# Optimization experiments

Measured on AMD Instinct MI355X. Metric: run time of the kernel, lower is better.

Reference implementation:

```python
import jax, jax.numpy as jnp
import numpy as np

K_SIZES = (3, 9)          # per-level local window sizes (both < 13)
K_NUM = tuple((k * k - 1) // 2 for k in K_SIZES)  # topk sizes: (4, 40)
BN_EPS = 1e-5


def _make_local_ids(W, patch_id, k):
    """Replicates get_local_index (k<13 branch): wrap-around kxk window minus center."""
    r = k // 2
    out = []
    for i in patch_id:
        i = int(i)
        ix, iy = i // W, i % W
        wx = np.zeros(W)
        wy = np.zeros(W)
        for j in range(-r, r + 1):
            wx[(ix + j) % W] = 1.0
            wy[(iy + j) % W] = 1.0
        wgt = (wy[None, :] * wx[:, None]).reshape(-1)  # row-major: idx = x*W + y
        wgt[i] = 0.0
        out.append(np.nonzero(wgt)[0])
    return np.stack(out).astype(np.int64)  # [N, k*k-1]


def setup_inputs() -> dict:
    key = jax.random.key(0)
    ks = jax.random.split(key, 8)
    B = 8
    feat0 = jax.random.normal(ks[0], (B, 512, 8, 8), jnp.float32)
    feat1 = jax.random.normal(ks[1], (B, 64, 128, 128), jnp.float32)
    rng = np.random.default_rng(0)
    patch_id0 = rng.permutation(8 * 8)[:64]
    patch_id1 = rng.permutation(128 * 128)[:512]
    local_id0 = _make_local_ids(8, patch_id0, K_SIZES[0])    # [64, 8]
    local_id1 = _make_local_ids(128, patch_id1, K_SIZES[1])  # [512, 80]
    s = 0.02
    return dict(
        feat0=feat0, feat1=feat1,
        W1=jax.random.normal(ks[2], (1024, 512), jnp.float32) * s,
        b1=jnp.zeros((1024,), jnp.float32),
        gamma=jnp.ones((1024,), jnp.float32),
        beta=jnp.zeros((1024,), jnp.float32),
        W2=jax.random.normal(ks[3], (256, 1024), jnp.float32) * s,
        b2=jnp.zeros((256,), jnp.float32),
        W3=jax.random.normal(ks[4], (256, 64), jnp.float32) * s,
        b3=jnp.zeros((256,), jnp.float32),
        W4=jax.random.normal(ks[5], (256, 256), jnp.float32) * s,
        b4=jnp.zeros((256,), jnp.float32),
        patch_id0=jnp.asarray(patch_id0, jnp.int64 if jax.config.jax_enable_x64 else jnp.int32),
        patch_id1=jnp.asarray(patch_id1, jnp.int64 if jax.config.jax_enable_x64 else jnp.int32),
        local_id0=jnp.asarray(local_id0, jnp.int64 if jax.config.jax_enable_x64 else jnp.int32),
        local_id1=jnp.asarray(local_id1, jnp.int64 if jax.config.jax_enable_x64 else jnp.int32),
        patch_size=128,
    )


def _sample(feat, patch_id, local_id, k_num):
    """gather local patches -> cosine sim vs center -> topk -> gather winners."""
    B, C, H, W = feat.shape
    fr = jnp.transpose(feat, (0, 2, 3, 1)).reshape(B, H * W, C)  # [B, HW, C]
    norm = jnp.linalg.norm(fr, axis=-1, keepdims=True)
    xn = fr / jnp.maximum(norm, 1e-12)                 # F.normalize(dim=-1)
    loc = xn[:, local_id]                              # [B, N, L, C]
    cen = xn[:, patch_id]                              # [B, N, C]
    sim = jnp.einsum('bnlc,bnc->bnl', loc, cen)        # [B, N, L]
    _, top = jax.lax.top_k(sim, k_num)                 # [B, N, k]
    N, L = local_id.shape
    top = top.reshape(B * N, k_num, 1)
    x_loc = fr[:, local_id].reshape(B * N, L, C)
    x_loc = jnp.take_along_axis(x_loc, jnp.broadcast_to(top, (B * N, k_num, C)), axis=1)
    x_cen = fr[:, patch_id].reshape(B * N, 1, C)
    return jnp.concatenate([x_cen, x_loc], axis=1)     # [B*N, 1+k, C]


def reference(feat0, feat1, W1, b1, gamma, beta, W2, b2, W3, b3, W4, b4,
              patch_id0, patch_id1, local_id0, local_id1, patch_size):
    # level 0: h == patch_size // 16 -> adaptive_avg_pool over (1+k) axis, then mlp1
    x0 = _sample(feat0, patch_id0, local_id0, K_NUM[0])  # [B*N0, 1+k0, 512]
    x0 = x0.mean(axis=1)                                 # adaptive_avg_pool2d -> (1, dim)
    h = x0 @ W1.T + b1
    mu = h.mean(axis=0)
    var = h.var(axis=0)                                  # BatchNorm1d (training stats)
    h = (h - mu) / jnp.sqrt(var + BN_EPS) * gamma + beta
    out0 = jax.nn.relu(h) @ W2.T + b2                    # [B*N0, 256]

    # level 1: h == patch_size -> mlp2 per (center+neighbors) row, then l2norm
    x1 = _sample(feat1, patch_id1, local_id1, K_NUM[1])  # [B*N1, 1+k1, 64]
    BN1, M, C1 = x1.shape
    y = x1.reshape(-1, C1)
    y = jax.nn.relu(y @ W3.T + b3) @ W4.T + b4           # [B*N1*(1+k1), 256]
    y = y / (jnp.linalg.norm(y, axis=1, keepdims=True) + 1e-7)  # Normalize(2)
    out1 = y.reshape(BN1, M, -1)                         # [B*N1, 1+k1, 256]
    return out0, out1
```

## Files before the change

kernel.cpp:

```cpp
#include <hip/hip_runtime.h>
#include <math.h>

typedef _Float16 f16x8 __attribute__((ext_vector_type(8)));
typedef float f32x4 __attribute__((ext_vector_type(4)));


__global__ __launch_bounds__(256) void k_wprep(
    const float* __restrict__ W3, const float* __restrict__ W4,
    unsigned short* __restrict__ PB3h, unsigned short* __restrict__ PB3l,
    unsigned short* __restrict__ PB4h, unsigned short* __restrict__ PB4l)
{
    const int e = blockIdx.x * 256 + threadIdx.x;
    if (e < 16384) {
        const int j = e & 7, l = (e >> 3) & 63, ks = (e >> 9) & 1, nt = e >> 10;
        const int n = nt * 16 + (l & 15);
        const int k = ks * 32 + (l >> 4) * 8 + j;
        const float w = W3[n * 64 + k];
        const _Float16 hi = (_Float16)w;
        const _Float16 lo = (_Float16)(w - (float)hi);
        ((_Float16*)PB3h)[e] = hi;
        ((_Float16*)PB3l)[e] = lo;
    }
    {
        const int j = e & 7, l = (e >> 3) & 63, ks = (e >> 9) & 7, nt = e >> 12;
        const int n = nt * 16 + (l & 15);
        const int k = ks * 32 + (l >> 4) * 8 + j;
        const float w = W4[n * 256 + k];
        const _Float16 hi = (_Float16)w;
        const _Float16 lo = (_Float16)(w - (float)hi);
        ((_Float16*)PB4h)[e] = hi;
        ((_Float16*)PB4l)[e] = lo;
    }
}

__global__ __launch_bounds__(256) void k_transpose1(
    const float* __restrict__ feat1, float* __restrict__ featT)
{
    __shared__ float tile[64][65];
    const int b = blockIdx.y;
    const int p0 = blockIdx.x * 64;
    const int tid = threadIdx.x;
    const float* fb = feat1 + (size_t)b * 64 * 16384;
    float* ft = featT + (size_t)b * 16384 * 64;
    #pragma unroll
    for (int it = 0; it < 16; ++it) {
        const int e = it * 256 + tid;
        const int c = e >> 6, p = e & 63;
        tile[p][c] = fb[(size_t)c * 16384 + p0 + p];
    }
    __syncthreads();
    #pragma unroll
    for (int it = 0; it < 16; ++it) {
        const int e = it * 256 + tid;
        const int p = e >> 6, c = e & 63;
        ft[(size_t)(p0 + p) * 64 + c] = tile[p][c];
    }
}

__global__ __launch_bounds__(128) void k_sims1T(
    const float* __restrict__ featT, const int* __restrict__ patch_id1,
    const int* __restrict__ local_id1, int* __restrict__ idx)
{
    __shared__ float cen[64];
    __shared__ double sims[80];
    __shared__ double cnorm;

    const int row = blockIdx.x;
    const int b = row >> 9;
    const int n = row & 511;
    const int tid = threadIdx.x;
    const float* ft = featT + (size_t)b * 16384 * 64;
    const int pid = patch_id1[n];
    const int* lids = local_id1 + n * 80;

    if (tid < 64) cen[tid] = ft[(size_t)pid * 64 + tid];
    __syncthreads();

    if (tid < 64) {
        double v = (double)cen[tid];
        double s = v * v;
        for (int o = 32; o > 0; o >>= 1) s += __shfl_down(s, o);
        if (tid == 0) { s = sqrt(s); cnorm = (s < 1e-12) ? 1e-12 : s; }
    }
    __syncthreads();

    if (tid < 80) {
        const float4* rp = (const float4*)(ft + (size_t)lids[tid] * 64);
        double d = 0.0, q = 0.0;
        #pragma unroll
        for (int k = 0; k < 16; ++k) {
            const float4 v4 = rp[k];
            double v;
            v = (double)v4.x; d += v * (double)cen[4*k+0]; q += v*v;
            v = (double)v4.y; d += v * (double)cen[4*k+1]; q += v*v;
            v = (double)v4.z; d += v * (double)cen[4*k+2]; q += v*v;
            v = (double)v4.w; d += v * (double)cen[4*k+3]; q += v*v;
        }
        double nl = sqrt(q); if (nl < 1e-12) nl = 1e-12;
        sims[tid] = d / (nl * cnorm);
    }
    __syncthreads();

    if (tid < 80) {
        const double s = sims[tid];
        int rank = 0;
        for (int j = 0; j < 80; ++j) {
            const double sj = sims[j];
            rank += (sj > s) || (sj == s && j < tid);
        }
        if (rank < 40) idx[row * 41 + 1 + rank] = lids[tid];
    }
    if (tid == 0) idx[row * 41] = pid;
}

__global__ __launch_bounds__(128) void k_sims1(
    const float* __restrict__ feat1, const int* __restrict__ patch_id1,
    const int* __restrict__ local_id1, int* __restrict__ idx)
{
    __shared__ float cen[64];
    __shared__ double sims[80];
    __shared__ double cnorm;

    const int row = blockIdx.x;
    const int b = row >> 9;
    const int n = row & 511;
    const int tid = threadIdx.x;
    const float* fb = feat1 + (size_t)b * 64 * 16384;
    const int pid = patch_id1[n];
    const int* lids = local_id1 + n * 80;

    if (tid < 64) cen[tid] = fb[(size_t)tid * 16384 + pid];
    __syncthreads();

    if (tid < 64) {
        double v = (double)cen[tid];
        double s = v * v;
        for (int o = 32; o > 0; o >>= 1) s += __shfl_down(s, o);
        if (tid == 0) { s = sqrt(s); cnorm = (s < 1e-12) ? 1e-12 : s; }
    }
    __syncthreads();

    if (tid < 80) {
        const int lpix = lids[tid];
        double d = 0.0, q = 0.0;
        for (int c = 0; c < 64; ++c) {
            double v = (double)fb[(size_t)c * 16384 + lpix];
            d += v * (double)cen[c];
            q += v * v;
        }
        double nl = sqrt(q); if (nl < 1e-12) nl = 1e-12;
        sims[tid] = d / (nl * cnorm);
    }
    __syncthreads();

    if (tid < 80) {
        const double s = sims[tid];
        int rank = 0;
        for (int j = 0; j < 80; ++j) {
            const double sj = sims[j];
            rank += (sj > s) || (sj == s && j < tid);
        }
        if (rank < 40) idx[row * 41 + 1 + rank] = lids[tid];
    }
    if (tid == 0) idx[row * 41] = pid;
}

__global__ __launch_bounds__(256) void k_mlp_mfma(
    const float* __restrict__ featb,
    const unsigned short* __restrict__ PB3h, const unsigned short* __restrict__ PB3l,
    const unsigned short* __restrict__ PB4h, const unsigned short* __restrict__ PB4l,
    const float* __restrict__ b3, const float* __restrict__ b4,
    float* __restrict__ ybuf)
{
    __shared__ _Float16 XH[32][72];
    __shared__ _Float16 XL[32][72];
    __shared__ float T1[32][260];
    __shared__ float rsums[2][2][16];

    const int tid = threadIdx.x;
    const int blk = blockIdx.x;
    const int img = blk >> 9;
    const int p0 = (blk & 511) * 32;
    const float* fb = featb + (size_t)img * 64 * 16384;
    float* yb = ybuf + (size_t)img * (size_t)(16384 * 256);

    {
        const int p = tid & 31;
        const int cg = tid >> 5;
        #pragma unroll
        for (int k = 0; k < 8; ++k) {
            const int c = cg * 8 + k;
            const float v = fb[(size_t)c * 16384 + p0 + p];
            const _Float16 hi = (_Float16)v;
            XH[p][c] = hi;
            XL[p][c] = (_Float16)(v - (float)hi);
        }
    }
    __syncthreads();

    const int lane = tid & 63;
    const int w = tid >> 6;
    const int mt = w & 1;
    const int nh = w >> 1;
    const int lrow = lane & 15;
    const int kblk = lane >> 4;

    {
        f16x8 ah[2], al[2];
        #pragma unroll
        for (int ks = 0; ks < 2; ++ks) {
            ah[ks] = *(const f16x8*)&XH[mt*16 + lrow][ks*32 + kblk*8];
            al[ks] = *(const f16x8*)&XL[mt*16 + lrow][ks*32 + kblk*8];
        }
        const f16x8* B3H = (const f16x8*)PB3h;
        const f16x8* B3L = (const f16x8*)PB3l;
        #pragma unroll
        for (int t = 0; t < 8; ++t) {
            const int nt = nh*8 + t;
            f32x4 acc = {0.f, 0.f, 0.f, 0.f};
            #pragma unroll
            for (int ks = 0; ks < 2; ++ks) {
                const f16x8 bh = B3H[(nt*2 + ks)*64 + lane];
                const f16x8 bl = B3L[(nt*2 + ks)*64 + lane];
                acc = __builtin_amdgcn_mfma_f32_16x16x32_f16(al[ks], bh, acc, 0, 0, 0);
                acc = __builtin_amdgcn_mfma_f32_16x16x32_f16(ah[ks], bl, acc, 0, 0, 0);
                acc = __builtin_amdgcn_mfma_f32_16x16x32_f16(ah[ks], bh, acc, 0, 0, 0);
            }
            const float bias = b3[nt*16 + lrow];
            #pragma unroll
            for (int r = 0; r < 4; ++r)
                T1[mt*16 + kblk*4 + r][nt*16 + lrow] = fmaxf(acc[r] + bias, 0.f);
        }
    }
    __syncthreads();

    f32x4 acc2[8];
    #pragma unroll
    for (int t = 0; t < 8; ++t) acc2[t] = (f32x4){0.f, 0.f, 0.f, 0.f};
    {
        const f16x8* B4H = (const f16x8*)PB4h;
        const f16x8* B4L = (const f16x8*)PB4l;
        #pragma unroll 2
        for (int ks = 0; ks < 8; ++ks) {
            float a[8];
            *(float4*)&a[0] = *(const float4*)&T1[mt*16 + lrow][ks*32 + kblk*8];
            *(float4*)&a[4] = *(const float4*)&T1[mt*16 + lrow][ks*32 + kblk*8 + 4];
            f16x8 ah2, al2;
            #pragma unroll
            for (int j = 0; j < 8; ++j) {
                const _Float16 hi = (_Float16)a[j];
                ah2[j] = hi;
                al2[j] = (_Float16)(a[j] - (float)hi);
            }
            #pragma unroll
            for (int t = 0; t < 8; ++t) {
                const int nt = nh*8 + t;
                const f16x8 bh = B4H[(nt*8 + ks)*64 + lane];
                const f16x8 bl = B4L[(nt*8 + ks)*64 + lane];
                acc2[t] = __builtin_amdgcn_mfma_f32_16x16x32_f16(al2, bh, acc2[t], 0, 0, 0);
                acc2[t] = __builtin_amdgcn_mfma_f32_16x16x32_f16(ah2, bl, acc2[t], 0, 0, 0);
                acc2[t] = __builtin_amdgcn_mfma_f32_16x16x32_f16(ah2, bh, acc2[t], 0, 0, 0);
            }
        }
    }
    float p[4] = {0.f, 0.f, 0.f, 0.f};
    #pragma unroll
    for (int t = 0; t < 8; ++t) {
        const float bias = b4[(nh*8 + t)*16 + lrow];
        #pragma unroll
        for (int r = 0; r < 4; ++r) {
            acc2[t][r] += bias;
            p[r] += acc2[t][r] * acc2[t][r];
        }
    }
    #pragma unroll
    for (int r = 0; r < 4; ++r)
        for (int o = 1; o < 16; o <<= 1) p[r] += __shfl_xor(p[r], o);
    if (lrow == 0) {
        #pragma unroll
        for (int r = 0; r < 4; ++r) rsums[mt][nh][kblk*4 + r] = p[r];
    }
    __syncthreads();
    float inv[4];
    #pragma unroll
    for (int r = 0; r < 4; ++r) {
        const float s = rsums[mt][0][kblk*4 + r] + rsums[mt][1][kblk*4 + r];
        inv[r] = 1.f / (sqrtf(s) + 1e-7f);
    }
    #pragma unroll
    for (int t = 0; t < 8; ++t) {
        const int col = (nh*8 + t)*16 + lrow;
        #pragma unroll
        for (int r = 0; r < 4; ++r)
            yb[(size_t)(p0 + mt*16 + kblk*4 + r) * 256 + col] = acc2[t][r] * inv[r];
    }
}

__global__ __launch_bounds__(256) void k_mlp_pix2(
    const float* __restrict__ featb,
    const float* __restrict__ W3T, const float* __restrict__ b3,
    const float* __restrict__ W4T, const float* __restrict__ b4,
    float* __restrict__ ybuf, int ybufStride)
{
    __shared__ __align__(16) float xs[32 * 68];
    __shared__ __align__(16) float t1s[32 * 256];

    const int tid = threadIdx.x;
    const int blk = blockIdx.x;
    const int img = blk >> 9;
    const int p0 = (blk & 511) * 32;
    const float* fb = featb + (size_t)img * 64 * 16384;
    float* yb = ybuf + (size_t)img * (size_t)ybufStride;

    {
        const int p = tid & 31;
        const int cg = tid >> 5;
        #pragma unroll
        for (int k = 0; k < 8; ++k) {
            const int c = cg * 8 + k;
            xs[p * 68 + c] = fb[(size_t)c * 16384 + p0 + p];
        }
    }
    __syncthreads();

    const int jg = tid & 63;
    const int g = tid >> 6;
    const int j0 = jg * 4;
    const int mb = g * 8;

    {
        float acc[8][4];
        #pragma unroll
        for (int r = 0; r < 8; ++r) {
            acc[r][0] = 0.f; acc[r][1] = 0.f; acc[r][2] = 0.f; acc[r][3] = 0.f;
        }
        const float4* Wf = (const float4*)W3T;
        const float4* xsf = (const float4*)xs;
        #pragma unroll 4
        for (int cq = 0; cq < 16; ++cq) {
            const float4 wA = Wf[(cq * 4 + 0) * 64 + jg];
            const float4 wB = Wf[(cq * 4 + 1) * 64 + jg];
            const float4 wC = Wf[(cq * 4 + 2) * 64 + jg];
            const float4 wD = Wf[(cq * 4 + 3) * 64 + jg];
            #pragma unroll
            for (int r = 0; r < 8; ++r) {
                const float4 x4 = xsf[(mb + r) * 17 + cq];
                acc[r][0] += x4.x*wA.x + x4.y*wB.x + x4.z*wC.x + x4.w*wD.x;
                acc[r][1] += x4.x*wA.y + x4.y*wB.y + x4.z*wC.y + x4.w*wD.y;
                acc[r][2] += x4.x*wA.z + x4.y*wB.z + x4.z*wC.z + x4.w*wD.z;
                acc[r][3] += x4.x*wA.w + x4.y*wB.w + x4.z*wC.w + x4.w*wD.w;
            }
        }
        const float bb0 = b3[j0], bb1 = b3[j0+1], bb2 = b3[j0+2], bb3 = b3[j0+3];
        #pragma unroll
        for (int r = 0; r < 8; ++r) {
            float4 o4;
            o4.x = fmaxf(acc[r][0] + bb0, 0.f);
            o4.y = fmaxf(acc[r][1] + bb1, 0.f);
            o4.z = fmaxf(acc[r][2] + bb2, 0.f);
            o4.w = fmaxf(acc[r][3] + bb3, 0.f);
            *(float4*)&t1s[(mb + r) * 256 + j0] = o4;
        }
    }
    __syncthreads();

    {
        float acc[8][4];
        #pragma unroll
        for (int r = 0; r < 8; ++r) {
            acc[r][0] = 0.f; acc[r][1] = 0.f; acc[r][2] = 0.f; acc[r][3] = 0.f;
        }
        const float4* Wf = (const float4*)W4T;
        const float4* t1f = (const float4*)t1s;
        #pragma unroll 2
        for (int kq = 0; kq < 64; ++kq) {
            const float4 wA = Wf[(kq * 4 + 0) * 64 + jg];
            const float4 wB = Wf[(kq * 4 + 1) * 64 + jg];
            const float4 wC = Wf[(kq * 4 + 2) * 64 + jg];
            const float4 wD = Wf[(kq * 4 + 3) * 64 + jg];
            #pragma unroll
            for (int r = 0; r < 8; ++r) {
                const float4 t4 = t1f[(mb + r) * 64 + kq];
                acc[r][0] += t4.x*wA.x + t4.y*wB.x + t4.z*wC.x + t4.w*wD.x;
                acc[r][1] += t4.x*wA.y + t4.y*wB.y + t4.z*wC.y + t4.w*wD.y;
                acc[r][2] += t4.x*wA.z + t4.y*wB.z + t4.z*wC.z + t4.w*wD.z;
                acc[r][3] += t4.x*wA.w + t4.y*wB.w + t4.z*wC.w + t4.w*wD.w;
            }
        }
        const float bb0 = b4[j0], bb1 = b4[j0+1], bb2 = b4[j0+2], bb3 = b4[j0+3];
        #pragma unroll
        for (int r = 0; r < 8; ++r) {
            const float y0 = acc[r][0] + bb0;
            const float y1 = acc[r][1] + bb1;
            const float y2 = acc[r][2] + bb2;
            const float y3 = acc[r][3] + bb3;
            float p = y0*y0 + y1*y1 + y2*y2 + y3*y3;
            for (int o = 1; o < 64; o <<= 1) p += __shfl_xor(p, o);
            const float inv = 1.f / (sqrtf(p) + 1e-7f);
            float4 o4 = make_float4(y0*inv, y1*inv, y2*inv, y3*inv);
            *(float4*)&yb[(size_t)(p0 + mb + r) * 256 + j0] = o4;
        }
    }
}

__global__ __launch_bounds__(256) void k_wtrans(
    const float* __restrict__ W3, const float* __restrict__ W4,
    float* __restrict__ W3T, float* __restrict__ W4T)
{
    const int t = threadIdx.x;
    const int j = blockIdx.x;
    W4T[(size_t)t * 256 + j] = W4[(size_t)j * 256 + t];
    if (j < 64) W3T[(size_t)j * 256 + t] = W3[(size_t)t * 64 + j];
}

__global__ __launch_bounds__(256) void k_gather1(
    const float* __restrict__ ybuf, int ybufStride,
    const int* __restrict__ idxb, float* __restrict__ out1b)
{
    __shared__ int pix[41];
    const int bn = blockIdx.x;
    const int img = bn >> 9;
    const int tid = threadIdx.x;
    if (tid < 41) pix[tid] = idxb[bn * 41 + tid];
    __syncthreads();
    const float4* yb4 = (const float4*)(ybuf + (size_t)img * (size_t)ybufStride);
    float4* o4 = (float4*)(out1b + (size_t)bn * 41 * 256);
    for (int e = tid; e < 41 * 64; e += 256) {
        const int mi = e >> 6, j4 = e & 63;
        o4[mi * 64 + j4] = yb4[pix[mi] * 64 + j4];
    }
}

__global__ __launch_bounds__(256) void k_branch1(
    const float* __restrict__ feat1, const int* __restrict__ patch_id1,
    const int* __restrict__ local_id1, const float* __restrict__ W3,
    const float* __restrict__ b3, const float* __restrict__ W4,
    const float* __restrict__ b4, float* __restrict__ out1)
{
    __shared__ __align__(16) float xs[44 * 64];
    __shared__ __align__(16) float t1s[44 * 256];
    __shared__ double sims[80];
    __shared__ int winners[40];
    __shared__ float cen[64];
    __shared__ double cnorm;

    const int row = blockIdx.x;
    const int b = row >> 9;
    const int n = row & 511;
    const int tid = threadIdx.x;
    const float* fb = feat1 + (size_t)b * 64 * 16384;
    const int pid = patch_id1[n];
    const int* lids = local_id1 + n * 80;

    if (tid < 64) cen[tid] = fb[(size_t)tid * 16384 + pid];
    __syncthreads();

    if (tid < 64) {
        double v = (double)cen[tid];
        double s = v * v;
        for (int o = 32; o > 0; o >>= 1) s += __shfl_down(s, o);
        if (tid == 0) { s = sqrt(s); cnorm = (s < 1e-12) ? 1e-12 : s; }
    }
    __syncthreads();

    if (tid < 80) {
        const int lpix = lids[tid];
        double d = 0.0, q = 0.0;
        for (int c = 0; c < 64; ++c) {
            double v = (double)fb[(size_t)c * 16384 + lpix];
            d += v * (double)cen[c];
            q += v * v;
        }
        double nl = sqrt(q); if (nl < 1e-12) nl = 1e-12;
        sims[tid] = d / (nl * cnorm);
    }
    __syncthreads();

    if (tid < 80) {
        const double s = sims[tid];
        int rank = 0;
        for (int j = 0; j < 80; ++j) {
            const double sj = sims[j];
            rank += (sj > s) || (sj == s && j < tid);
        }
        if (rank < 40) winners[rank] = tid;
    }
    __syncthreads();

    for (int m = tid; m < 44 * 64; m += 256) {
        const int mi = m >> 6, c = m & 63;
        float v;
        if (mi >= 1 && mi <= 40) v = fb[(size_t)c * 16384 + lids[winners[mi - 1]]];
        else v = cen[c];
        xs[m] = v;
    }
    __syncthreads();

    const int jg = tid & 63;
    const int g = tid >> 6;
    const int j0 = jg * 4;
    const int mb = g * 11;

    {
        float acc[11][4];
        #pragma unroll
        for (int r = 0; r < 11; ++r) {
            acc[r][0] = 0.f; acc[r][1] = 0.f; acc[r][2] = 0.f; acc[r][3] = 0.f;
        }
        const float4* W3f = (const float4*)W3;
        const float4* xsf = (const float4*)xs;
        #pragma unroll 4
        for (int c4 = 0; c4 < 16; ++c4) {
            const float4 w0 = W3f[(j0 + 0) * 16 + c4];
            const float4 w1 = W3f[(j0 + 1) * 16 + c4];
            const float4 w2 = W3f[(j0 + 2) * 16 + c4];
            const float4 w3 = W3f[(j0 + 3) * 16 + c4];
            #pragma unroll
            for (int r = 0; r < 11; ++r) {
                const float4 x4 = xsf[(mb + r) * 16 + c4];
                acc[r][0] += x4.x*w0.x + x4.y*w0.y + x4.z*w0.z + x4.w*w0.w;
                acc[r][1] += x4.x*w1.x + x4.y*w1.y + x4.z*w1.z + x4.w*w1.w;
                acc[r][2] += x4.x*w2.x + x4.y*w2.y + x4.z*w2.z + x4.w*w2.w;
                acc[r][3] += x4.x*w3.x + x4.y*w3.y + x4.z*w3.z + x4.w*w3.w;
            }
        }
        const float bb0 = b3[j0], bb1 = b3[j0+1], bb2 = b3[j0+2], bb3 = b3[j0+3];
        #pragma unroll
        for (int r = 0; r < 11; ++r) {
            float4 o4;
            o4.x = fmaxf(acc[r][0] + bb0, 0.f);
            o4.y = fmaxf(acc[r][1] + bb1, 0.f);
            o4.z = fmaxf(acc[r][2] + bb2, 0.f);
            o4.w = fmaxf(acc[r][3] + bb3, 0.f);
            *(float4*)&t1s[(mb + r) * 256 + j0] = o4;
        }
    }
    __syncthreads();

    {
        float acc[11][4];
        #pragma unroll
        for (int r = 0; r < 11; ++r) {
            acc[r][0] = 0.f; acc[r][1] = 0.f; acc[r][2] = 0.f; acc[r][3] = 0.f;
        }
        const float4* W4f = (const float4*)W4;
        const float4* t1f = (const float4*)t1s;
        #pragma unroll 2
        for (int j4 = 0; j4 < 64; ++j4) {
            const float4 w0 = W4f[(j0 + 0) * 64 + j4];
            const float4 w1 = W4f[(j0 + 1) * 64 + j4];
            const float4 w2 = W4f[(j0 + 2) * 64 + j4];
            const float4 w3 = W4f[(j0 + 3) * 64 + j4];
            #pragma unroll
            for (int r = 0; r < 11; ++r) {
                const float4 t4 = t1f[(mb + r) * 64 + j4];
                acc[r][0] += t4.x*w0.x + t4.y*w0.y + t4.z*w0.z + t4.w*w0.w;
                acc[r][1] += t4.x*w1.x + t4.y*w1.y + t4.z*w1.z + t4.w*w1.w;
                acc[r][2] += t4.x*w2.x + t4.y*w2.y + t4.z*w2.z + t4.w*w2.w;
                acc[r][3] += t4.x*w3.x + t4.y*w3.y + t4.z*w3.z + t4.w*w3.w;
            }
        }
        const float bb0 = b4[j0], bb1 = b4[j0+1], bb2 = b4[j0+2], bb3 = b4[j0+3];
        #pragma unroll
        for (int r = 0; r < 11; ++r) {
            const float y0 = acc[r][0] + bb0;
            const float y1 = acc[r][1] + bb1;
            const float y2 = acc[r][2] + bb2;
            const float y3 = acc[r][3] + bb3;
            float p = y0*y0 + y1*y1 + y2*y2 + y3*y3;
            for (int o = 1; o < 64; o <<= 1) p += __shfl_xor(p, o);
            const float inv = 1.f / (sqrtf(p) + 1e-7f);
            const int mi = mb + r;
            if (mi < 41) {
                float4 o4 = make_float4(y0*inv, y1*inv, y2*inv, y3*inv);
                *(float4*)&out1[((size_t)row * 41 + mi) * 256 + j0] = o4;
            }
        }
    }
}

__global__ __launch_bounds__(64) void k_sample0(
    const float* __restrict__ feat0, const int* __restrict__ patch_id0,
    const int* __restrict__ local_id0, float* __restrict__ x0m)
{
    __shared__ float cen[512];
    __shared__ float loc[8][512];
    __shared__ double sims[8];
    __shared__ int winners[4];
    __shared__ double cnorm;

    const int row = blockIdx.x;
    const int b = row >> 6;
    const int n = row & 63;
    const int t = threadIdx.x;
    const float* fb = feat0 + (size_t)b * 512 * 64;
    const int pid = patch_id0[n];

    for (int c = t; c < 512; c += 64) cen[c] = fb[(size_t)c * 64 + pid];
    for (int l = 0; l < 8; ++l) {
        const int lp = local_id0[n * 8 + l];
        for (int c = t; c < 512; c += 64) loc[l][c] = fb[(size_t)c * 64 + lp];
    }
    __syncthreads();

    double cs = 0.0;
    for (int c = t; c < 512; c += 64) { double v = (double)cen[c]; cs += v * v; }
    for (int o = 32; o > 0; o >>= 1) cs += __shfl_down(cs, o);
    if (t == 0) { cs = sqrt(cs); cnorm = (cs < 1e-12) ? 1e-12 : cs; }
    __syncthreads();

    for (int l = 0; l < 8; ++l) {
        double d = 0.0, q = 0.0;
        for (int c = t; c < 512; c += 64) {
            double v = (double)loc[l][c];
            d += v * (double)cen[c];
            q += v * v;
        }
        for (int o = 32; o > 0; o >>= 1) { d += __shfl_down(d, o); q += __shfl_down(q, o); }
        if (t == 0) {
            double nl = sqrt(q); if (nl < 1e-12) nl = 1e-12;
            sims[l] = d / (nl * cnorm);
        }
    }
    __syncthreads();

    if (t < 8) {
        const double s = sims[t];
        int rank = 0;
        for (int j = 0; j < 8; ++j) {
            const double sj = sims[j];
            rank += (sj > s) || (sj == s && j < t);
        }
        if (rank < 4) winners[rank] = t;
    }
    __syncthreads();

    for (int c = t; c < 512; c += 64) {
        float a = cen[c];
        for (int r = 0; r < 4; ++r) a += loc[winners[r]][c];
        x0m[(size_t)row * 512 + c] = a * 0.2f;
    }
}

__global__ __launch_bounds__(128) void k_gemm1(
    const float* __restrict__ x, const float* __restrict__ W1,
    const float* __restrict__ b1, float* __restrict__ h)
{
    __shared__ __align__(16) float xsr[8 * 512];
    const int i0 = blockIdx.y * 8;
    const int tid = threadIdx.x;
    const int j0 = blockIdx.x * 512 + tid * 4;

    const float4* xg = (const float4*)(x + (size_t)i0 * 512);
    float4* xl = (float4*)xsr;
    #pragma unroll
    for (int e = 0; e < 8; ++e) xl[e * 128 + tid] = xg[e * 128 + tid];
    __syncthreads();

    float acc[8][4];
    #pragma unroll
    for (int r = 0; r < 8; ++r) {
        acc[r][0] = 0.f; acc[r][1] = 0.f; acc[r][2] = 0.f; acc[r][3] = 0.f;
    }
    const float4* W1f = (const float4*)W1;
    const float4* xf  = (const float4*)xsr;
    #pragma unroll 4
    for (int c4 = 0; c4 < 128; ++c4) {
        const float4 w0 = W1f[(size_t)(j0 + 0) * 128 + c4];
        const float4 w1 = W1f[(size_t)(j0 + 1) * 128 + c4];
        const float4 w2 = W1f[(size_t)(j0 + 2) * 128 + c4];
        const float4 w3 = W1f[(size_t)(j0 + 3) * 128 + c4];
        #pragma unroll
        for (int r = 0; r < 8; ++r) {
            const float4 x4 = xf[r * 128 + c4];
            acc[r][0] += x4.x*w0.x + x4.y*w0.y + x4.z*w0.z + x4.w*w0.w;
            acc[r][1] += x4.x*w1.x + x4.y*w1.y + x4.z*w1.z + x4.w*w1.w;
            acc[r][2] += x4.x*w2.x + x4.y*w2.y + x4.z*w2.z + x4.w*w2.w;
            acc[r][3] += x4.x*w3.x + x4.y*w3.y + x4.z*w3.z + x4.w*w3.w;
        }
    }
    const float bb0 = b1[j0], bb1 = b1[j0+1], bb2 = b1[j0+2], bb3 = b1[j0+3];
    #pragma unroll
    for (int r = 0; r < 8; ++r) {
        float4 o4 = make_float4(acc[r][0] + bb0, acc[r][1] + bb1,
                                acc[r][2] + bb2, acc[r][3] + bb3);
        *(float4*)&h[(size_t)(i0 + r) * 1024 + j0] = o4;
    }
}

__global__ __launch_bounds__(64) void k_bnstats(
    const float* __restrict__ h, float* __restrict__ mu, float* __restrict__ rstd)
{
    const int j = blockIdx.x;
    const int t = threadIdx.x;
    float s = 0.f, ss = 0.f;
    for (int i = t; i < 512; i += 64) {
        const float v = h[(size_t)i * 1024 + j];
        s += v; ss += v * v;
    }
    for (int o = 32; o > 0; o >>= 1) { s += __shfl_down(s, o); ss += __shfl_down(ss, o); }
    if (t == 0) {
        const float m = s * (1.f / 512.f);
        const float var = ss * (1.f / 512.f) - m * m;
        mu[j] = m;
        rstd[j] = rsqrtf(var + 1e-5f);
    }
}

__global__ __launch_bounds__(256) void k_bnapply(
    float* __restrict__ h, const float* __restrict__ mu, const float* __restrict__ rstd,
    const float* __restrict__ gamma, const float* __restrict__ beta)
{
    const int e = blockIdx.x * 256 + threadIdx.x;
    const int jb = (e & 255) * 4;
    float4 v = ((float4*)h)[e];
    v.x = fmaxf((v.x - mu[jb+0]) * rstd[jb+0] * gamma[jb+0] + beta[jb+0], 0.f);
    v.y = fmaxf((v.y - mu[jb+1]) * rstd[jb+1] * gamma[jb+1] + beta[jb+1], 0.f);
    v.z = fmaxf((v.z - mu[jb+2]) * rstd[jb+2] * gamma[jb+2] + beta[jb+2], 0.f);
    v.w = fmaxf((v.w - mu[jb+3]) * rstd[jb+3] * gamma[jb+3] + beta[jb+3], 0.f);
    ((float4*)h)[e] = v;
}

__global__ __launch_bounds__(256) void k_gemm2(
    const float* __restrict__ h, const float* __restrict__ W2,
    const float* __restrict__ b2, float* __restrict__ out0)
{
    __shared__ __align__(16) float hs[8 * 1024];
    const int i0 = blockIdx.x * 8;
    const int j = threadIdx.x;

    const float4* hg = (const float4*)(h + (size_t)i0 * 1024);
    float4* hl = (float4*)hs;
    #pragma unroll
    for (int e = 0; e < 8; ++e) hl[e * 256 + j] = hg[e * 256 + j];
    __syncthreads();

    float acc[8];
    #pragma unroll
    for (int r = 0; r < 8; ++r) acc[r] = 0.f;
    const float4* wr = (const float4*)(W2 + (size_t)j * 1024);
    const float4* hf = (const float4*)hs;
    #pragma unroll 4
    for (int k4 = 0; k4 < 256; ++k4) {
        const float4 w = wr[k4];
        #pragma unroll
        for (int r = 0; r < 8; ++r) {
            const float4 a = hf[r * 256 + k4];
            acc[r] += a.x*w.x + a.y*w.y + a.z*w.z + a.w*w.w;
        }
    }
    const float bb = b2[j];
    #pragma unroll
    for (int r = 0; r < 8; ++r)
        out0[(size_t)(i0 + r) * 256 + j] = acc[r] + bb;
}

extern "C" void kernel_launch(void* const* d_in, const int* in_sizes, int n_in,
                              void* d_out, int out_size, void* d_ws, size_t ws_size,
                              hipStream_t stream) {
    const float* feat0 = (const float*)d_in[0];
    const float* feat1 = (const float*)d_in[1];
    const float* W1    = (const float*)d_in[2];
    const float* b1    = (const float*)d_in[3];
    const float* gamma = (const float*)d_in[4];
    const float* beta  = (const float*)d_in[5];
    const float* W2    = (const float*)d_in[6];
    const float* b2    = (const float*)d_in[7];
    const float* W3    = (const float*)d_in[8];
    const float* b3    = (const float*)d_in[9];
    const float* W4    = (const float*)d_in[10];
    const float* b4    = (const float*)d_in[11];
    const int* patch_id0 = (const int*)d_in[12];
    const int* patch_id1 = (const int*)d_in[13];
    const int* local_id0 = (const int*)d_in[14];
    const int* local_id1 = (const int*)d_in[15];

    float* out0 = (float*)d_out;
    float* out1 = out0 + 512 * 256;

    float* ws    = (float*)d_ws;
    float* x0m   = ws;
    float* h     = ws + 262144;
    float* mu    = ws + 786432;
    float* rstd  = ws + 787456;
    int*   idx   = (int*)(ws + 788480);
    float* W3T   = ws + 956416;
    float* W4T   = ws + 972800;
    unsigned short* PB3h = (unsigned short*)(ws + 956416);
    unsigned short* PB3l = PB3h + 16384;
    unsigned short* PB4h = PB3l + 16384;
    unsigned short* PB4l = PB4h + 65536;
    float* ybuf  = ws + 1038336;

    const int YB_STRIDE = 16384 * 256;

    const size_t NEED_C = (size_t)(1038336 + 4194304) * 4;
    const size_t NEED_B = (size_t)(1038336 + 4194304 + 8388608) * 4;
    const size_t NEED_A = (size_t)(1038336 + 33554432 + 8388608) * 4;

    if (ws_size >= NEED_A) {
        float* featT = ws + 1038336 + 33554432;
        k_wprep<<<256, 256, 0, stream>>>(W3, W4, PB3h, PB3l, PB4h, PB4l);
        k_transpose1<<<dim3(256, 8), 256, 0, stream>>>(feat1, featT);
        k_sims1T<<<4096, 128, 0, stream>>>(featT, patch_id1, local_id1, idx);
        k_mlp_mfma<<<4096, 256, 0, stream>>>(feat1, PB3h, PB3l, PB4h, PB4l,
                                             b3, b4, ybuf);
        k_gather1<<<4096, 256, 0, stream>>>(ybuf, YB_STRIDE, idx, out1);
    } else if (ws_size >= NEED_C) {
        k_wtrans<<<256, 256, 0, stream>>>(W3, W4, W3T, W4T);
        if (ws_size >= NEED_B) {
            float* featT = ws + 1038336 + 4194304;
            k_transpose1<<<dim3(256, 8), 256, 0, stream>>>(feat1, featT);
            k_sims1T<<<4096, 128, 0, stream>>>(featT, patch_id1, local_id1, idx);
        } else {
            k_sims1<<<4096, 128, 0, stream>>>(feat1, patch_id1, local_id1, idx);
        }
        for (int b = 0; b < 8; ++b) {
            k_mlp_pix2<<<512, 256, 0, stream>>>(
                feat1 + (size_t)b * 64 * 16384, W3T, b3, W4T, b4, ybuf, 0);
            k_gather1<<<512, 256, 0, stream>>>(
                ybuf, 0, idx + (size_t)b * 512 * 41,
                out1 + (size_t)b * 512 * 41 * 256);
        }
    } else {
        k_branch1<<<4096, 256, 0, stream>>>(feat1, patch_id1, local_id1,
                                            W3, b3, W4, b4, out1);
    }

    k_sample0<<<512, 64, 0, stream>>>(feat0, patch_id0, local_id0, x0m);
    k_gemm1<<<dim3(2, 64), 128, 0, stream>>>(x0m, W1, b1, h);
    k_bnstats<<<1024, 64, 0, stream>>>(h, mu, rstd);
    k_bnapply<<<512, 256, 0, stream>>>(h, mu, rstd, gamma, beta);
    k_gemm2<<<64, 256, 0, stream>>>(h, W2, b2, out0);
}
```

Before: 612.0 us.

## Fuse MLP with scatter to outputs via inverse pixel index, drop ybuf

Builds a per-pixel inverse index (count via atomics in the similarity kernel, prefix scan, slot fill) so the MLP kernel can write each normalized pixel row directly to every output row that references it. This removes the full-image intermediate buffer write and the separate gather pass. The hidden activations are stored pre-split into f16 hi/lo in shared memory instead of being converted per k-step. It adds atomics, extra small kernels, and scattered output stores, and lowers the workspace requirement of the fast path.

```diff
diff --git a/kernel.cpp b/kernel.cpp
--- a/kernel.cpp
+++ b/kernel.cpp
@@ -57,9 +57,16 @@
     }
 }
 
+__global__ __launch_bounds__(256) void k_zero(unsigned* __restrict__ p, int n)
+{
+    const int i = blockIdx.x * 256 + threadIdx.x;
+    if (i < n) p[i] = 0u;
+}
+
 __global__ __launch_bounds__(128) void k_sims1T(
     const float* __restrict__ featT, const int* __restrict__ patch_id1,
-    const int* __restrict__ local_id1, int* __restrict__ idx)
+    const int* __restrict__ local_id1, int* __restrict__ idx,
+    unsigned* __restrict__ cnt)
 {
     __shared__ float cen[64];
     __shared__ double sims[80];
@@ -108,9 +115,210 @@
             const double sj = sims[j];
             rank += (sj > s) || (sj == s && j < tid);
         }
-        if (rank < 40) idx[row * 41 + 1 + rank] = lids[tid];
-    }
-    if (tid == 0) idx[row * 41] = pid;
+        if (rank < 40) {
+            idx[row * 41 + 1 + rank] = lids[tid];
+            atomicAdd(&cnt[b * 16384 + lids[tid]], 1u);
+        }
+    }
+    if (tid == 0) {
+        idx[row * 41] = pid;
+        atomicAdd(&cnt[b * 16384 + pid], 1u);
+    }
+}
+
+__global__ __launch_bounds__(256) void k_scan(
+    const unsigned* __restrict__ cnt, unsigned* __restrict__ off,
+    unsigned* __restrict__ cursor)
+{
+    __shared__ unsigned ssum[256];
+    const int img = blockIdx.x;
+    const int t = threadIdx.x;
+    const unsigned* c = cnt + img * 16384;
+    unsigned s = 0;
+    for (int i = 0; i < 64; ++i) s += c[t * 64 + i];
+    ssum[t] = s;
+    __syncthreads();
+    if (t == 0) {
+        unsigned run = 0;
+        for (int i = 0; i < 256; ++i) { const unsigned v = ssum[i]; ssum[i] = run; run += v; }
+    }
+    __syncthreads();
+    unsigned run = ssum[t];
+    unsigned* o  = off + img * 16384;
+    unsigned* cu = cursor + img * 16384;
+    for (int i = 0; i < 64; ++i) {
+        const int p = t * 64 + i;
+        o[p] = run; cu[p] = run;
+        run += c[p];
+    }
+}
+
+__global__ __launch_bounds__(256) void k_fill(
+    const int* __restrict__ idx, unsigned* __restrict__ cursor,
+    int* __restrict__ slots)
+{
+    const int e = blockIdx.x * 256 + threadIdx.x;
+    if (e >= 4096 * 41) return;
+    const int row = e / 41;
+    const int img = row >> 9;
+    const int pix = idx[e];
+    const unsigned pos = atomicAdd(&cursor[img * 16384 + pix], 1u);
+    slots[img * 20992 + pos] = e;
+}
+
+__global__ __launch_bounds__(256, 4) void k_mlp_fused(
+    const float* __restrict__ featb,
+    const unsigned short* __restrict__ PB3h, const unsigned short* __restrict__ PB3l,
+    const unsigned short* __restrict__ PB4h, const unsigned short* __restrict__ PB4l,
+    const float* __restrict__ b3, const float* __restrict__ b4,
+    const unsigned* __restrict__ cnt, const unsigned* __restrict__ off,
+    const int* __restrict__ slots, float* __restrict__ out1)
+{
+    __shared__ __align__(16) unsigned char smem[33792];
+    _Float16 (*XH)[72]  = (_Float16(*)[72])smem;
+    _Float16 (*XL)[72]  = (_Float16(*)[72])(smem + 4608);
+    _Float16 (*TH)[264] = (_Float16(*)[264])smem;
+    _Float16 (*TL)[264] = (_Float16(*)[264])(smem + 16896);
+    __shared__ float rsums[2][2][16];
+
+    const int tid = threadIdx.x;
+    const int blk = blockIdx.x;
+    const int img = blk >> 9;
+    const int p0 = (blk & 511) * 32;
+    const float* fb = featb + (size_t)img * 64 * 16384;
+
+    {
+        const int p = tid & 31;
+        const int cg = tid >> 5;
+        #pragma unroll
+        for (int k = 0; k < 8; ++k) {
+            const int c = cg * 8 + k;
+            const float v = fb[(size_t)c * 16384 + p0 + p];
+            const _Float16 hi = (_Float16)v;
+            XH[p][c] = hi;
+            XL[p][c] = (_Float16)(v - (float)hi);
+        }
+    }
+    __syncthreads();
+
+    const int lane = tid & 63;
+    const int w = tid >> 6;
+    const int mt = w & 1;
+    const int nh = w >> 1;
+    const int lrow = lane & 15;
+    const int kblk = lane >> 4;
+
+    f16x8 ah[2], al[2];
+    #pragma unroll
+    for (int ks = 0; ks < 2; ++ks) {
+        ah[ks] = *(const f16x8*)&XH[mt*16 + lrow][ks*32 + kblk*8];
+        al[ks] = *(const f16x8*)&XL[mt*16 + lrow][ks*32 + kblk*8];
+    }
+    __syncthreads();
+
+    {
+        const f16x8* B3H = (const f16x8*)PB3h;
+        const f16x8* B3L = (const f16x8*)PB3l;
+        #pragma unroll
+        for (int t = 0; t < 8; ++t) {
+            const int nt = nh*8 + t;
+            const f16x8 bh0 = B3H[(nt*2 + 0)*64 + lane];
+            const f16x8 bl0 = B3L[(nt*2 + 0)*64 + lane];
+            const f16x8 bh1 = B3H[(nt*2 + 1)*64 + lane];
+            const f16x8 bl1 = B3L[(nt*2 + 1)*64 + lane];
+            f32x4 acc = {0.f, 0.f, 0.f, 0.f};
+            acc = __builtin_amdgcn_mfma_f32_16x16x32_f16(al[0], bh0, acc, 0, 0, 0);
+            acc = __builtin_amdgcn_mfma_f32_16x16x32_f16(ah[0], bl0, acc, 0, 0, 0);
+            acc = __builtin_amdgcn_mfma_f32_16x16x32_f16(ah[0], bh0, acc, 0, 0, 0);
+            acc = __builtin_amdgcn_mfma_f32_16x16x32_f16(al[1], bh1, acc, 0, 0, 0);
+            acc = __builtin_amdgcn_mfma_f32_16x16x32_f16(ah[1], bl1, acc, 0, 0, 0);
+            acc = __builtin_amdgcn_mfma_f32_16x16x32_f16(ah[1], bh1, acc, 0, 0, 0);
+            const float bias = b3[nt*16 + lrow];
+            #pragma unroll
+            for (int r = 0; r < 4; ++r) {
+                const float tv = fmaxf(acc[r] + bias, 0.f);
+                const _Float16 hi = (_Float16)tv;
+                TH[mt*16 + kblk*4 + r][nt*16 + lrow] = hi;
+                TL[mt*16 + kblk*4 + r][nt*16 + lrow] = (_Float16)(tv - (float)hi);
+            }
+        }
+    }
+    __syncthreads();
+
+    f32x4 acc2[8];
+    #pragma unroll
+    for (int t = 0; t < 8; ++t) acc2[t] = (f32x4){0.f, 0.f, 0.f, 0.f};
+    {
+        const f16x8* B4H = (const f16x8*)PB4h;
+        const f16x8* B4L = (const f16x8*)PB4l;
+        #pragma unroll 2
+        for (int ks = 0; ks < 8; ++ks) {
+            const f16x8 a2h = *(const f16x8*)&TH[mt*16 + lrow][ks*32 + kblk*8];
+            const f16x8 a2l = *(const f16x8*)&TL[mt*16 + lrow][ks*32 + kblk*8];
+            #pragma unroll
+            for (int th = 0; th < 2; ++th) {
+                f16x8 bh[4], bl[4];
+                #pragma unroll
+                for (int q = 0; q < 4; ++q) {
+                    const int nt = nh*8 + th*4 + q;
+                    bh[q] = B4H[(nt*8 + ks)*64 + lane];
+                    bl[q] = B4L[(nt*8 + ks)*64 + lane];
+                }
+                #pragma unroll
+                for (int q = 0; q < 4; ++q) {
+                    const int t = th*4 + q;
+                    acc2[t] = __builtin_amdgcn_mfma_f32_16x16x32_f16(a2l, bh[q], acc2[t], 0, 0, 0);
+                    acc2[t] = __builtin_amdgcn_mfma_f32_16x16x32_f16(a2h, bl[q], acc2[t], 0, 0, 0);
+                    acc2[t] = __builtin_amdgcn_mfma_f32_16x16x32_f16(a2h, bh[q], acc2[t], 0, 0, 0);
+                }
+            }
+        }
+    }
+
+    float p[4] = {0.f, 0.f, 0.f, 0.f};
+    #pragma unroll
+    for (int t = 0; t < 8; ++t) {
+        const float bias = b4[(nh*8 + t)*16 + lrow];
+        #pragma unroll
+        for (int r = 0; r < 4; ++r) {
+            acc2[t][r] += bias;
+            p[r] += acc2[t][r] * acc2[t][r];
+        }
+    }
+    #pragma unroll
+    for (int r = 0; r < 4; ++r)
+        for (int o = 1; o < 16; o <<= 1) p[r] += __shfl_xor(p[r], o);
+    if (lrow == 0) {
+        #pragma unroll
+        for (int r = 0; r < 4; ++r) rsums[mt][nh][kblk*4 + r] = p[r];
+    }
+    __syncthreads();
+    float inv[4];
+    #pragma unroll
+    for (int r = 0; r < 4; ++r) {
+        const float s = rsums[mt][0][kblk*4 + r] + rsums[mt][1][kblk*4 + r];
+        inv[r] = 1.f / (sqrtf(s) + 1e-7f);
+    }
+
+    const unsigned* cntp = cnt + img * 16384;
+    const unsigned* offp = off + img * 16384;
+    const int* slotp = slots + img * 20992;
+    #pragma unroll
+    for (int r = 0; r < 4; ++r) {
+        const int row = mt*16 + kblk*4 + r;
+        const int pix = p0 + row;
+        const unsigned deg = cntp[pix];
+        const unsigned st = offp[pix];
+        float y[8];
+        #pragma unroll
+        for (int t = 0; t < 8; ++t) y[t] = acc2[t][r] * inv[r];
+        for (unsigned s = 0; s < deg; ++s) {
+            const int e = slotp[st + s];
+            float* dst = out1 + (size_t)e * 256 + nh*128 + lrow;
+            #pragma unroll
+            for (int t = 0; t < 8; ++t) dst[t*16] = y[t];
+        }
+    }
 }
 
 __global__ __launch_bounds__(128) void k_sims1(
@@ -163,137 +371,6 @@
         if (rank < 40) idx[row * 41 + 1 + rank] = lids[tid];
     }
     if (tid == 0) idx[row * 41] = pid;
-}
-
-__global__ __launch_bounds__(256) void k_mlp_mfma(
-    const float* __restrict__ featb,
-    const unsigned short* __restrict__ PB3h, const unsigned short* __restrict__ PB3l,
-    const unsigned short* __restrict__ PB4h, const unsigned short* __restrict__ PB4l,
-    const float* __restrict__ b3, const float* __restrict__ b4,
-    float* __restrict__ ybuf)
-{
-    __shared__ _Float16 XH[32][72];
-    __shared__ _Float16 XL[32][72];
-    __shared__ float T1[32][260];
-    __shared__ float rsums[2][2][16];
-
-    const int tid = threadIdx.x;
-    const int blk = blockIdx.x;
-    const int img = blk >> 9;
-    const int p0 = (blk & 511) * 32;
-    const float* fb = featb + (size_t)img * 64 * 16384;
-    float* yb = ybuf + (size_t)img * (size_t)(16384 * 256);
-
-    {
-        const int p = tid & 31;
-        const int cg = tid >> 5;
-        #pragma unroll
-        for (int k = 0; k < 8; ++k) {
-            const int c = cg * 8 + k;
-            const float v = fb[(size_t)c * 16384 + p0 + p];
-            const _Float16 hi = (_Float16)v;
-            XH[p][c] = hi;
-            XL[p][c] = (_Float16)(v - (float)hi);
-        }
-    }
-    __syncthreads();
-
-    const int lane = tid & 63;
-    const int w = tid >> 6;
-    const int mt = w & 1;
-    const int nh = w >> 1;
-    const int lrow = lane & 15;
-    const int kblk = lane >> 4;
-
-    {
-        f16x8 ah[2], al[2];
-        #pragma unroll
-        for (int ks = 0; ks < 2; ++ks) {
-            ah[ks] = *(const f16x8*)&XH[mt*16 + lrow][ks*32 + kblk*8];
-            al[ks] = *(const f16x8*)&XL[mt*16 + lrow][ks*32 + kblk*8];
-        }
-        const f16x8* B3H = (const f16x8*)PB3h;
-        const f16x8* B3L = (const f16x8*)PB3l;
-        #pragma unroll
-        for (int t = 0; t < 8; ++t) {
-            const int nt = nh*8 + t;
-            f32x4 acc = {0.f, 0.f, 0.f, 0.f};
-            #pragma unroll
-            for (int ks = 0; ks < 2; ++ks) {
-                const f16x8 bh = B3H[(nt*2 + ks)*64 + lane];
-                const f16x8 bl = B3L[(nt*2 + ks)*64 + lane];
-                acc = __builtin_amdgcn_mfma_f32_16x16x32_f16(al[ks], bh, acc, 0, 0, 0);
-                acc = __builtin_amdgcn_mfma_f32_16x16x32_f16(ah[ks], bl, acc, 0, 0, 0);
-                acc = __builtin_amdgcn_mfma_f32_16x16x32_f16(ah[ks], bh, acc, 0, 0, 0);
-            }
-            const float bias = b3[nt*16 + lrow];
-            #pragma unroll
-            for (int r = 0; r < 4; ++r)
-                T1[mt*16 + kblk*4 + r][nt*16 + lrow] = fmaxf(acc[r] + bias, 0.f);
-        }
-    }
-    __syncthreads();
-
-    f32x4 acc2[8];
-    #pragma unroll
-    for (int t = 0; t < 8; ++t) acc2[t] = (f32x4){0.f, 0.f, 0.f, 0.f};
-    {
-        const f16x8* B4H = (const f16x8*)PB4h;
-        const f16x8* B4L = (const f16x8*)PB4l;
-        #pragma unroll 2
-        for (int ks = 0; ks < 8; ++ks) {
-            float a[8];
-            *(float4*)&a[0] = *(const float4*)&T1[mt*16 + lrow][ks*32 + kblk*8];
-            *(float4*)&a[4] = *(const float4*)&T1[mt*16 + lrow][ks*32 + kblk*8 + 4];
-            f16x8 ah2, al2;
-            #pragma unroll
-            for (int j = 0; j < 8; ++j) {
-                const _Float16 hi = (_Float16)a[j];
-                ah2[j] = hi;
-                al2[j] = (_Float16)(a[j] - (float)hi);
-            }
-            #pragma unroll
-            for (int t = 0; t < 8; ++t) {
-                const int nt = nh*8 + t;
-                const f16x8 bh = B4H[(nt*8 + ks)*64 + lane];
-                const f16x8 bl = B4L[(nt*8 + ks)*64 + lane];
-                acc2[t] = __builtin_amdgcn_mfma_f32_16x16x32_f16(al2, bh, acc2[t], 0, 0, 0);
-                acc2[t] = __builtin_amdgcn_mfma_f32_16x16x32_f16(ah2, bl, acc2[t], 0, 0, 0);
-                acc2[t] = __builtin_amdgcn_mfma_f32_16x16x32_f16(ah2, bh, acc2[t], 0, 0, 0);
-            }
-        }
-    }
-    float p[4] = {0.f, 0.f, 0.f, 0.f};
-    #pragma unroll
-    for (int t = 0; t < 8; ++t) {
-        const float bias = b4[(nh*8 + t)*16 + lrow];
-        #pragma unroll
-        for (int r = 0; r < 4; ++r) {
-            acc2[t][r] += bias;
-            p[r] += acc2[t][r] * acc2[t][r];
-        }
-    }
-    #pragma unroll
-    for (int r = 0; r < 4; ++r)
-        for (int o = 1; o < 16; o <<= 1) p[r] += __shfl_xor(p[r], o);
-    if (lrow == 0) {
-        #pragma unroll
-        for (int r = 0; r < 4; ++r) rsums[mt][nh][kblk*4 + r] = p[r];
-    }
-    __syncthreads();
-    float inv[4];
-    #pragma unroll
-    for (int r = 0; r < 4; ++r) {
-        const float s = rsums[mt][0][kblk*4 + r] + rsums[mt][1][kblk*4 + r];
-        inv[r] = 1.f / (sqrtf(s) + 1e-7f);
-    }
-    #pragma unroll
-    for (int t = 0; t < 8; ++t) {
-        const int col = (nh*8 + t)*16 + lrow;
-        #pragma unroll
-        for (int r = 0; r < 4; ++r)
-            yb[(size_t)(p0 + mt*16 + kblk*4 + r) * 256 + col] = acc2[t][r] * inv[r];
-    }
 }
 
 __global__ __launch_bounds__(256) void k_mlp_pix2(
@@ -790,31 +867,30 @@
     unsigned short* PB3l = PB3h + 16384;
     unsigned short* PB4h = PB3l + 16384;
     unsigned short* PB4l = PB4h + 65536;
+    unsigned* cnt    = (unsigned*)(ws + 1038336);
+    unsigned* off    = (unsigned*)(ws + 1169408);
+    unsigned* cursor = (unsigned*)(ws + 1300480);
+    int*      slots  = (int*)(ws + 1431552);
+    float*    featTA = ws + 1599488;
     float* ybuf  = ws + 1038336;
-
     const int YB_STRIDE = 16384 * 256;
 
+    const size_t NEED_A = (size_t)(1599488 + 8388608) * 4;
+    const size_t NEED_B = (size_t)(1038336 + 4194304 + 8388608) * 4;
     const size_t NEED_C = (size_t)(1038336 + 4194304) * 4;
-    const size_t NEED_B = (size_t)(1038336 + 4194304 + 8388608) * 4;
-    const size_t NEED_A = (size_t)(1038336 + 33554432 + 8388608) * 4;
 
     if (ws_size >= NEED_A) {
-        float* featT = ws + 1038336 + 33554432;
         k_wprep<<<256, 256, 0, stream>>>(W3, W4, PB3h, PB3l, PB4h, PB4l);
-        k_transpose1<<<dim3(256, 8), 256, 0, stream>>>(feat1, featT);
-        k_sims1T<<<4096, 128, 0, stream>>>(featT, patch_id1, local_id1, idx);
-        k_mlp_mfma<<<4096, 256, 0, stream>>>(feat1, PB3h, PB3l, PB4h, PB4l,
-                                             b3, b4, ybuf);
-        k_gather1<<<4096, 256, 0, stream>>>(ybuf, YB_STRIDE, idx, out1);
+        k_transpose1<<<dim3(256, 8), 256, 0, stream>>>(feat1, featTA);
+        k_zero<<<512, 256, 0, stream>>>(cnt, 131072);
+        k_sims1T<<<4096, 128, 0, stream>>>(featTA, patch_id1, local_id1, idx, cnt);
+        k_scan<<<8, 256, 0, stream>>>(cnt, off, cursor);
+        k_fill<<<656, 256, 0, stream>>>(idx, cursor, slots);
+        k_mlp_fused<<<4096, 256, 0, stream>>>(feat1, PB3h, PB3l, PB4h, PB4l,
+                                              b3, b4, cnt, off, slots, out1);
     } else if (ws_size >= NEED_C) {
         k_wtrans<<<256, 256, 0, stream>>>(W3, W4, W3T, W4T);
-        if (ws_size >= NEED_B) {
-            float* featT = ws + 1038336 + 4194304;
-            k_transpose1<<<dim3(256, 8), 256, 0, stream>>>(feat1, featT);
-            k_sims1T<<<4096, 128, 0, stream>>>(featT, patch_id1, local_id1, idx);
-        } else {
-            k_sims1<<<4096, 128, 0, stream>>>(feat1, patch_id1, local_id1, idx);
-        }
+        k_sims1<<<4096, 128, 0, stream>>>(feat1, patch_id1, local_id1, idx);
         for (int b = 0; b < 8; ++b) {
             k_mlp_pix2<<<512, 256, 0, stream>>>(
                 feat1 + (size_t)b * 64 * 16384, W3T, b3, W4T, b4, ybuf, 0);
```

New measurement: 581.9 us. 4.9% less time.
